# Kernel optimization log

Hardware: AMD Instinct MI355X
Metric: run time of the kernel (lower is better)

The kernel has to match this reference:

```python
import jax, jax.numpy as jnp
import numpy as np

TOKENS = 8192
DIM = 4096
N_EXPERTS = 256
TOPK = 8
N_GROUPS = 8
TOPK_GROUPS = 4
ROUTE_SCALE = 2.5


def setup_inputs() -> dict:
    key = jax.random.key(0)
    k1, k2, k3 = jax.random.split(key, 3)
    x = jax.random.normal(k1, (TOKENS, DIM), dtype=jnp.float32)
    W = jax.random.normal(k2, (N_EXPERTS, DIM), dtype=jnp.float32) * (DIM ** -0.5)
    bias = jax.random.normal(k3, (N_EXPERTS,), dtype=jnp.float32) * 0.01
    return {"x": x, "W": W, "bias": bias}


def reference(x, W, bias):
    T = x.shape[0]
    # linear scoring: [T, E]
    logits = jnp.einsum("td,ed->te", x, W)
    scores = jax.nn.sigmoid(logits)  # score_func == 'sigmoid'
    original_scores = scores
    s = scores + bias  # bias-corrected scores used only for routing
    # group-limited routing: [T, G, E/G]
    sg = s.reshape(T, N_GROUPS, -1)
    # bias is not None -> group score = sum of top-2 within each group
    group_scores = jax.lax.top_k(sg, 2)[0].sum(axis=-1)  # [T, G]
    gidx = jax.lax.top_k(group_scores, TOPK_GROUPS)[1]  # [T, topk_groups]
    mask = jnp.zeros((T, N_GROUPS), dtype=s.dtype).at[
        jnp.arange(T)[:, None], gidx
    ].set(1.0)
    s_masked = (sg * mask[:, :, None]).reshape(T, -1)  # [T, E]
    # final top-k over masked scores
    indices = jax.lax.top_k(s_masked, TOPK)[1]  # [T, topk] int32
    weights = jnp.take_along_axis(original_scores, indices, axis=1)
    # sigmoid path: renormalize selected weights
    weights = weights / weights.sum(axis=-1, keepdims=True)
    weights = weights * ROUTE_SCALE
    return weights.astype(x.dtype), indices
```

## Files before the change

### kernel.cpp

```cpp
#include <hip/hip_runtime.h>
#include <math.h>

#define TOKENS 8192
#define DIM 4096
#define NEXP 256
#define TK 8
#define ROUTE_SCALE 2.5f
#define TH1 1e-5f
#define TH2 2e-5f

#define PITCH 40

typedef _Float16 half8 __attribute__((ext_vector_type(8)));
typedef float f4 __attribute__((ext_vector_type(4)));
union H8 { half8 v; int4 q; };

__global__ __launch_bounds__(256) void wsplit(const float* __restrict__ W,
                                              _Float16* __restrict__ Whp,
                                              _Float16* __restrict__ Wlp,
                                              float4* __restrict__ Wt4,
                                              int* __restrict__ flag_cnt) {
    int fi = blockIdx.x * 256 + threadIdx.x;
    if (fi == 0) *flag_cnt = 0;
    int lane = fi & 63;
    int kc = (fi >> 6) & 127;
    int et = fi >> 13;
    int e = et * 16 + (lane & 15);
    int k = kc * 32 + ((lane >> 4) << 3);
    const float* src = W + (size_t)e * DIM + k;
    float4 a = *(const float4*)src;
    float4 b = *(const float4*)(src + 4);
    int kq = kc * 8 + ((lane >> 4) << 1);
    Wt4[(size_t)kq * NEXP + e] = a;
    Wt4[(size_t)(kq + 1) * NEXP + e] = b;
    float f[8] = {a.x, a.y, a.z, a.w, b.x, b.y, b.z, b.w};
    H8 hh, hl;
#pragma unroll
    for (int j = 0; j < 8; j++) {
        float ws = f[j] * 256.0f;
        _Float16 h = (_Float16)ws;
        float r = ws - (float)h;
        hh.v[j] = h;
        hl.v[j] = (_Float16)(r * 2048.0f);
    }
    *(int4*)(Whp + (size_t)fi * 8) = hh.q;
    *(int4*)(Wlp + (size_t)fi * 8) = hl.q;
}

__global__ __launch_bounds__(256, 3) void score_gemm(const float* __restrict__ x,
                                                     const _Float16* __restrict__ Whp,
                                                     const _Float16* __restrict__ Wlp,
                                                     float* __restrict__ parts) {
    __shared__ __align__(16) _Float16 sAh[2][64 * PITCH];
    __shared__ __align__(16) _Float16 sAl[2][64 * PITCH];

    const int m0 = blockIdx.x * 64;
    const int nb = blockIdx.y;
    const int chunk = blockIdx.z;
    const int kcb = 43 * chunk;
    const int kce = kcb + (chunk == 2 ? 42 : 43);

    const int tid = threadIdx.x;
    const int lane = tid & 63;
    const int wave = tid >> 6;
    const int et0 = nb * 8 + wave * 2;

    const int srow = tid >> 2;
    const int scol = (tid & 3) * 8;
    const int sidx = srow * PITCH + scol;
    const float* xrow = x + (size_t)(m0 + srow) * DIM + scol;

    f4 accH[4][2], accC[4][2];
#pragma unroll
    for (int i = 0; i < 4; i++)
#pragma unroll
        for (int j = 0; j < 2; j++) { accH[i][j] = (f4)0.0f; accC[i][j] = (f4)0.0f; }

    float4 ra[2][2];
    half8 bh[2][2], bl[2][2];

#define LOADRAW(S, KC)                                                         \
    {                                                                          \
        const float* p_ = xrow + (size_t)(KC) * 32;                            \
        ra[S][0] = *(const float4*)p_;                                         \
        ra[S][1] = *(const float4*)(p_ + 4);                                   \
    }

#define CONV(S, B_)                                                            \
    {                                                                          \
        float f_[8] = {ra[S][0].x, ra[S][0].y, ra[S][0].z, ra[S][0].w,         \
                       ra[S][1].x, ra[S][1].y, ra[S][1].z, ra[S][1].w};        \
        H8 hh_, hl_;                                                           \
        _Pragma("unroll") for (int j_ = 0; j_ < 8; j_++) {                     \
            float xv_ = f_[j_] * 16.0f;                                        \
            _Float16 hv_ = (_Float16)xv_;                                      \
            float r_ = xv_ - (float)hv_;                                       \
            hh_.v[j_] = hv_;                                                   \
            hl_.v[j_] = (_Float16)(r_ * 2048.0f);                              \
        }                                                                      \
        *(int4*)&sAh[B_][sidx] = hh_.q;                                        \
        *(int4*)&sAl[B_][sidx] = hl_.q;                                        \
    }

#define BLOAD(P_, KC)                                                          \
    _Pragma("unroll") for (int nt_ = 0; nt_ < 2; nt_++) {                      \
        size_t o_ = ((size_t)((et0 + nt_) * 128 + (KC)) * 64 + lane) * 8;      \
        bh[P_][nt_] = *(const half8*)(Whp + o_);                               \
        bl[P_][nt_] = *(const half8*)(Wlp + o_);                               \
    }

#define MFMA_PHASE(P)                                                          \
    _Pragma("unroll") for (int mt_ = 0; mt_ < 4; mt_++) {                      \
        int ra_ = (mt_ * 16 + (lane & 15)) * PITCH + ((lane >> 4) << 3);       \
        half8 ah_ = *(const half8*)&sAh[P][ra_];                               \
        half8 al_ = *(const half8*)&sAl[P][ra_];                               \
        _Pragma("unroll") for (int nt_ = 0; nt_ < 2; nt_++) {                  \
            accH[mt_][nt_] = __builtin_amdgcn_mfma_f32_16x16x32_f16(           \
                ah_, bh[P][nt_], accH[mt_][nt_], 0, 0, 0);                     \
            accC[mt_][nt_] = __builtin_amdgcn_mfma_f32_16x16x32_f16(           \
                ah_, bl[P][nt_], accC[mt_][nt_], 0, 0, 0);                     \
            accC[mt_][nt_] = __builtin_amdgcn_mfma_f32_16x16x32_f16(           \
                al_, bh[P][nt_], accC[mt_][nt_], 0, 0, 0);                     \
        }                                                                      \
    }

#define BARRIER() asm volatile("s_waitcnt lgkmcnt(0)\n\ts_barrier" ::: "memory")

#define ITER(KC, P)                                                            \
    {                                                                          \
        if ((KC) + 1 < kce) { BLOAD(P ^ 1, (KC) + 1) }                         \
        if ((KC) + 2 < kce) { LOADRAW(P, (KC) + 2) }                           \
        MFMA_PHASE(P)                                                          \
        if ((KC) + 1 < kce) { CONV(P ^ 1, P ^ 1) }                             \
        BARRIER();                                                             \
    }

    LOADRAW(0, kcb)
    CONV(0, 0)
    LOADRAW(1, kcb + 1)
    BLOAD(0, kcb)
    BARRIER();

    int kc = kcb;
    while (kc + 2 <= kce) {
        ITER(kc, 0)
        ITER(kc + 1, 1)
        kc += 2;
    }
    if (kc < kce) { ITER(kc, 0) }

    float* pc = parts + (size_t)chunk * TOKENS * NEXP;
#pragma unroll
    for (int mt = 0; mt < 4; mt++)
#pragma unroll
        for (int nt = 0; nt < 2; nt++) {
            int m = m0 + mt * 16 + ((lane >> 4) << 2);
            int e = (et0 + nt) * 16 + (lane & 15);
#pragma unroll
            for (int r = 0; r < 4; r++)
                pc[(size_t)(m + r) * NEXP + e] =
                    accH[mt][nt][r] + accC[mt][nt][r] * (1.0f / 2048.0f);
        }
#undef LOADRAW
#undef CONV
#undef BLOAD
#undef MFMA_PHASE
#undef BARRIER
#undef ITER
}

__global__ __launch_bounds__(256) void route_kernel(const float* __restrict__ parts,
                                                    const float* __restrict__ bias,
                                                    float* __restrict__ out_w,
                                                    float* __restrict__ out_i,
                                                    int* __restrict__ flag_cnt,
                                                    int* __restrict__ flag_list) {
    const int t = blockIdx.x * 4 + (threadIdx.x >> 6);
    const int l = threadIdx.x & 63;

    const float* p = parts + (size_t)t * NEXP + (l << 2);
    float4 q0 = *(const float4*)p;
    float4 q1 = *(const float4*)(p + (size_t)TOKENS * NEXP);
    float4 q2 = *(const float4*)(p + (size_t)2 * TOKENS * NEXP);
    float4 b4 = *(const float4*)&bias[l << 2];
    float sc[4], sb[4];
    {
        float lg0 = (q0.x + q1.x + q2.x) * (1.0f / 4096.0f);
        float lg1 = (q0.y + q1.y + q2.y) * (1.0f / 4096.0f);
        float lg2 = (q0.z + q1.z + q2.z) * (1.0f / 4096.0f);
        float lg3 = (q0.w + q1.w + q2.w) * (1.0f / 4096.0f);
        sc[0] = 1.0f / (1.0f + expf(-lg0));
        sc[1] = 1.0f / (1.0f + expf(-lg1));
        sc[2] = 1.0f / (1.0f + expf(-lg2));
        sc[3] = 1.0f / (1.0f + expf(-lg3));
        sb[0] = sc[0] + b4.x; sb[1] = sc[1] + b4.y;
        sb[2] = sc[2] + b4.z; sb[3] = sc[3] + b4.w;
    }

    float v1 = sb[0], v2 = -1e30f, v3 = -1e30f;
#pragma unroll
    for (int c = 1; c < 4; c++) {
        float xv = sb[c];
        if (xv > v1) { v3 = v2; v2 = v1; v1 = xv; }
        else if (xv > v2) { v3 = v2; v2 = xv; }
        else if (xv > v3) { v3 = xv; }
    }

#pragma unroll
    for (int m = 1; m < 8; m <<= 1) {
        float o1 = __shfl_xor(v1, m, 64);
        float o2 = __shfl_xor(v2, m, 64);
        float o3 = __shfl_xor(v3, m, 64);
        bool aw = (v1 >= o1);
        float A1 = aw ? v1 : o1, A2 = aw ? v2 : o2, A3 = aw ? v3 : o3;
        float B1 = aw ? o1 : v1, B2 = aw ? o2 : v2;
        float n2, n3;
        if (A2 >= B1) { n2 = A2; n3 = fmaxf(B1, A3); }
        else          { n2 = B1; n3 = fmaxf(A2, B2); }
        v1 = A1; v2 = n2; v3 = n3;
    }
    float gscore = v1 + v2;
    float gap23 = v2 - v3;
#pragma unroll
    for (int m = 8; m < 64; m <<= 1) gap23 = fminf(gap23, __shfl_xor(gap23, m, 64));

    float gs[8];
#pragma unroll
    for (int g = 0; g < 8; g++) gs[g] = __shfl(gscore, g << 3, 64);

    const int mygrp = l >> 3;
    int rank = 0;
#pragma unroll
    for (int g = 0; g < 8; g++) {
        bool better = (gs[g] > gscore) || (gs[g] == gscore && g < mygrp);
        rank += (g != mygrp && better) ? 1 : 0;
    }
    const bool sel = rank < 4;

    float minsel = 1e30f, maxuns = -1e30f;
#pragma unroll
    for (int g = 0; g < 8; g++) {
        int rg = 0;
#pragma unroll
        for (int g2 = 0; g2 < 8; g2++)
            rg += (g2 != g && ((gs[g2] > gs[g]) || (gs[g2] == gs[g] && g2 < g))) ? 1 : 0;
        if (rg < 4) minsel = fminf(minsel, gs[g]); else maxuns = fmaxf(maxuns, gs[g]);
    }
    float gap45 = minsel - maxuns;

    float cand[4];
#pragma unroll
    for (int c = 0; c < 4; c++) cand[c] = sel ? sb[c] : 0.0f;

    float wv[8], wi[8], vb[9];
    float wsum = 0.0f;
#pragma unroll
    for (int r = 0; r < 9; r++) {
        float v = cand[0];
        int idx = (l << 2);
#pragma unroll
        for (int c = 1; c < 4; c++) {
            if (cand[c] > v) { v = cand[c]; idx = (l << 2) + c; }
        }
#pragma unroll
        for (int m = 32; m >= 1; m >>= 1) {
            float ov = __shfl_xor(v, m, 64);
            int oi = __shfl_xor(idx, m, 64);
            if (ov > v || (ov == v && oi < idx)) { v = ov; idx = oi; }
        }
        vb[r] = v;
        if (r < 8) {
            const int cc = idx & 3;
            const bool own = (idx >> 2) == l;
            cand[0] = (own && cc == 0) ? -__builtin_inff() : cand[0];
            cand[1] = (own && cc == 1) ? -__builtin_inff() : cand[1];
            cand[2] = (own && cc == 2) ? -__builtin_inff() : cand[2];
            cand[3] = (own && cc == 3) ? -__builtin_inff() : cand[3];
            float tmp = (cc == 0) ? sc[0] : (cc == 1) ? sc[1] : (cc == 2) ? sc[2] : sc[3];
            float ws = __shfl(tmp, idx >> 2, 64);
            wv[r] = ws;
            wi[r] = (float)idx;
            wsum += ws;
        }
    }
    float mingap = 1e30f;
#pragma unroll
    for (int r = 0; r < 8; r++) mingap = fminf(mingap, vb[r] - vb[r + 1]);

    const float scale = ROUTE_SCALE / wsum;
    if (l == 0) {
        float* ow = out_w + (size_t)t * TK;
        float* oi = out_i + (size_t)t * TK;
#pragma unroll
        for (int r = 0; r < 8; r++) ow[r] = wv[r] * scale;
#pragma unroll
        for (int r = 0; r < 8; r++) oi[r] = wi[r];
        if (gap23 < TH1 || gap45 < TH2 || mingap < TH1) {
            int pos = atomicAdd(flag_cnt, 1);
            flag_list[pos] = t;
        }
    }
}

__global__ __launch_bounds__(256, 1) void fixup_kernel(const float* __restrict__ x,
                                                       const float4* __restrict__ Wt4,
                                                       const float* __restrict__ bias,
                                                       const int* __restrict__ flag_cnt,
                                                       const int* __restrict__ flag_list,
                                                       float* __restrict__ out_w,
                                                       float* __restrict__ out_i) {
    __shared__ float S[NEXP];
    __shared__ __align__(16) float sx[DIM];
    const int tid = threadIdx.x;

#define FILL(BUF, S_)                                                          \
    _Pragma("unroll") for (int q_ = 0; q_ < 8; q_++)                           \
        BUF[q_] = wt4r[(size_t)((S_) * 8 + q_) * NEXP];

#define CONSUME(BUF, S_)                                                       \
    {                                                                          \
        const float* xb_ = sx + (S_) * 32;                                     \
        _Pragma("unroll") for (int q_ = 0; q_ < 8; q_++) {                     \
            const float4 wv = BUF[q_];                                         \
            const float4 xv = *(const float4*)(xb_ + q_ * 4);                  \
            acc = fmaf(xv.x, wv.x, acc);                                       \
            acc = fmaf(xv.y, wv.y, acc);                                       \
            acc = fmaf(xv.z, wv.z, acc);                                       \
            acc = fmaf(xv.w, wv.w, acc);                                       \
        }                                                                      \
    }

    const int n = *flag_cnt;
    for (int i = blockIdx.x; i < n; i += gridDim.x) {
        const int t = flag_list[i];
        const float* xr = x + (size_t)t * DIM;
#pragma unroll
        for (int j = 0; j < 4; j++) {
            const int idx = (j * 256 + tid) * 4;
            *(float4*)&sx[idx] = *(const float4*)(xr + idx);
        }
        __syncthreads();

        const float4* wt4r = Wt4 + tid;
        float4 wb0[8], wb1[8], wb2[8], wb3[8];
        FILL(wb0, 0)
        FILL(wb1, 1)
        FILL(wb2, 2)
        FILL(wb3, 3)

        float acc = 0.0f;
        for (int c4 = 0; c4 < 31; c4++) {
            const int s = c4 * 4;
            CONSUME(wb0, s)
            FILL(wb0, s + 4)
            CONSUME(wb1, s + 1)
            FILL(wb1, s + 5)
            CONSUME(wb2, s + 2)
            FILL(wb2, s + 6)
            CONSUME(wb3, s + 3)
            FILL(wb3, s + 7)
        }
        CONSUME(wb0, 124)
        CONSUME(wb1, 125)
        CONSUME(wb2, 126)
        CONSUME(wb3, 127)

        S[tid] = 1.0f / (1.0f + expf(-acc));
        __syncthreads();
        if (tid < 64) {
            const int l = tid;
            float sc[4] = {S[4 * l], S[4 * l + 1], S[4 * l + 2], S[4 * l + 3]};
            float4 b4 = *(const float4*)&bias[4 * l];
            float sb[4] = {sc[0] + b4.x, sc[1] + b4.y, sc[2] + b4.z, sc[3] + b4.w};

            float h1 = fmaxf(sb[0], sb[1]), q1 = fminf(sb[0], sb[1]);
            float h2 = fmaxf(sb[2], sb[3]), q2 = fminf(sb[2], sb[3]);
            float m1 = fmaxf(h1, h2);
            float m2 = fmaxf(fminf(h1, h2), fmaxf(q1, q2));
#pragma unroll
            for (int m = 1; m < 8; m <<= 1) {
                float o1 = __shfl_xor(m1, m, 64);
                float o2 = __shfl_xor(m2, m, 64);
                float nm1 = fmaxf(m1, o1);
                float nm2 = fmaxf(fminf(m1, o1), fmaxf(m2, o2));
                m1 = nm1; m2 = nm2;
            }
            float gscore = m1 + m2;
            float gs[8];
#pragma unroll
            for (int g = 0; g < 8; g++) gs[g] = __shfl(gscore, g << 3, 64);
            const int mygrp = l >> 3;
            int rank = 0;
#pragma unroll
            for (int g = 0; g < 8; g++) {
                bool better = (gs[g] > gscore) || (gs[g] == gscore && g < mygrp);
                rank += (g != mygrp && better) ? 1 : 0;
            }
            const bool selg = rank < 4;
            float cand[4];
#pragma unroll
            for (int c = 0; c < 4; c++) cand[c] = selg ? sb[c] : 0.0f;
            float wv[8], wi[8];
            float wsum = 0.0f;
#pragma unroll
            for (int r = 0; r < 8; r++) {
                float v = cand[0];
                int idx = (l << 2);
#pragma unroll
                for (int c = 1; c < 4; c++) {
                    if (cand[c] > v) { v = cand[c]; idx = (l << 2) + c; }
                }
#pragma unroll
                for (int m = 32; m >= 1; m >>= 1) {
                    float ov = __shfl_xor(v, m, 64);
                    int oi = __shfl_xor(idx, m, 64);
                    if (ov > v || (ov == v && oi < idx)) { v = ov; idx = oi; }
                }
                const int cc = idx & 3;
                const bool own = (idx >> 2) == l;
                cand[0] = (own && cc == 0) ? -__builtin_inff() : cand[0];
                cand[1] = (own && cc == 1) ? -__builtin_inff() : cand[1];
                cand[2] = (own && cc == 2) ? -__builtin_inff() : cand[2];
                cand[3] = (own && cc == 3) ? -__builtin_inff() : cand[3];
                float tmp = (cc == 0) ? sc[0] : (cc == 1) ? sc[1] : (cc == 2) ? sc[2] : sc[3];
                float ws = __shfl(tmp, idx >> 2, 64);
                wv[r] = ws;
                wi[r] = (float)idx;
                wsum += ws;
            }
            const float scale = ROUTE_SCALE / wsum;
            if (l == 0) {
                float* ow = out_w + (size_t)t * TK;
                float* oi = out_i + (size_t)t * TK;
#pragma unroll
                for (int r = 0; r < 8; r++) ow[r] = wv[r] * scale;
#pragma unroll
                for (int r = 0; r < 8; r++) oi[r] = wi[r];
            }
        }
        __syncthreads();
    }
#undef FILL
#undef CONSUME
}

extern "C" void kernel_launch(void* const* d_in, const int* in_sizes, int n_in,
                              void* d_out, int out_size, void* d_ws, size_t ws_size,
                              hipStream_t stream) {
    const float* x = (const float*)d_in[0];
    const float* W = (const float*)d_in[1];
    const float* bias = (const float*)d_in[2];
    float* out = (float*)d_out;

    char* p = (char*)d_ws;
    float* parts = (float*)p;            p += (size_t)3 * TOKENS * NEXP * 4;
    _Float16* Whp = (_Float16*)p;        p += (size_t)NEXP * DIM * 2;
    _Float16* Wlp = (_Float16*)p;        p += (size_t)NEXP * DIM * 2;
    int* flag_cnt = (int*)p;
    int* flag_list = flag_cnt + 4;       p += 40960;
    float4* Wt4 = (float4*)p;

    wsplit<<<512, 256, 0, stream>>>(W, Whp, Wlp, Wt4, flag_cnt);

    dim3 gGemm(TOKENS / 64, 2, 3);
    score_gemm<<<gGemm, 256, 0, stream>>>(x, Whp, Wlp, parts);

    route_kernel<<<TOKENS / 4, 256, 0, stream>>>(parts, bias, out,
                                                 out + (size_t)TOKENS * TK,
                                                 flag_cnt, flag_list);
    fixup_kernel<<<256, 256, 0, stream>>>(x, Wt4, bias, flag_cnt, flag_list,
                                          out, out + (size_t)TOKENS * TK);
}
```

Measured before the change: 301.6 us.

## Cover all experts per GEMM block and batch four tokens in fixup

The score GEMM now uses 512-thread blocks whose 8 waves cover all 256 experts. Each x tile is loaded and split into fp16 hi/lo once per block instead of once per expert half, and the K dimension is split into 4 chunks of 32 rather than 3 uneven ones. The route kernel sums four partial buffers, which adds partial-sum memory traffic. The fixup kernel processes four flagged tokens per block, reusing each streamed W value across four dot products at the cost of more shared memory.

```diff
diff --git a/kernel.cpp b/kernel.cpp
--- a/kernel.cpp
+++ b/kernel.cpp
@@ -12,8 +12,10 @@
 #define PITCH 40
 
 typedef _Float16 half8 __attribute__((ext_vector_type(8)));
+typedef _Float16 half4 __attribute__((ext_vector_type(4)));
 typedef float f4 __attribute__((ext_vector_type(4)));
 union H8 { half8 v; int4 q; };
+union H4 { half4 v; int2 q; };
 
 __global__ __launch_bounds__(256) void wsplit(const float* __restrict__ W,
                                               _Float16* __restrict__ Whp,
@@ -47,7 +49,7 @@
     *(int4*)(Wlp + (size_t)fi * 8) = hl.q;
 }
 
-__global__ __launch_bounds__(256, 3) void score_gemm(const float* __restrict__ x,
+__global__ __launch_bounds__(512, 4) void score_gemm(const float* __restrict__ x,
                                                      const _Float16* __restrict__ Whp,
                                                      const _Float16* __restrict__ Wlp,
                                                      float* __restrict__ parts) {
@@ -55,18 +57,17 @@
     __shared__ __align__(16) _Float16 sAl[2][64 * PITCH];
 
     const int m0 = blockIdx.x * 64;
-    const int nb = blockIdx.y;
-    const int chunk = blockIdx.z;
-    const int kcb = 43 * chunk;
-    const int kce = kcb + (chunk == 2 ? 42 : 43);
+    const int chunk = blockIdx.y;
+    const int kcb = chunk * 32;
+    const int kce = kcb + 32;
 
     const int tid = threadIdx.x;
     const int lane = tid & 63;
     const int wave = tid >> 6;
-    const int et0 = nb * 8 + wave * 2;
-
-    const int srow = tid >> 2;
-    const int scol = (tid & 3) * 8;
+    const int et0 = wave * 2;
+
+    const int srow = tid >> 3;
+    const int scol = (tid & 7) * 4;
     const int sidx = srow * PITCH + scol;
     const float* xrow = x + (size_t)(m0 + srow) * DIM + scol;
 
@@ -76,30 +77,25 @@
 #pragma unroll
         for (int j = 0; j < 2; j++) { accH[i][j] = (f4)0.0f; accC[i][j] = (f4)0.0f; }
 
-    float4 ra[2][2];
+    float4 ra[2];
     half8 bh[2][2], bl[2][2];
 
 #define LOADRAW(S, KC)                                                         \
-    {                                                                          \
-        const float* p_ = xrow + (size_t)(KC) * 32;                            \
-        ra[S][0] = *(const float4*)p_;                                         \
-        ra[S][1] = *(const float4*)(p_ + 4);                                   \
-    }
+    { ra[S] = *(const float4*)(xrow + (size_t)(KC) * 32); }
 
 #define CONV(S, B_)                                                            \
     {                                                                          \
-        float f_[8] = {ra[S][0].x, ra[S][0].y, ra[S][0].z, ra[S][0].w,         \
-                       ra[S][1].x, ra[S][1].y, ra[S][1].z, ra[S][1].w};        \
-        H8 hh_, hl_;                                                           \
-        _Pragma("unroll") for (int j_ = 0; j_ < 8; j_++) {                     \
+        float f_[4] = {ra[S].x, ra[S].y, ra[S].z, ra[S].w};                    \
+        H4 hh_, hl_;                                                           \
+        _Pragma("unroll") for (int j_ = 0; j_ < 4; j_++) {                     \
             float xv_ = f_[j_] * 16.0f;                                        \
             _Float16 hv_ = (_Float16)xv_;                                      \
             float r_ = xv_ - (float)hv_;                                       \
             hh_.v[j_] = hv_;                                                   \
             hl_.v[j_] = (_Float16)(r_ * 2048.0f);                              \
         }                                                                      \
-        *(int4*)&sAh[B_][sidx] = hh_.q;                                        \
-        *(int4*)&sAl[B_][sidx] = hl_.q;                                        \
+        *(int2*)&sAh[B_][sidx] = hh_.q;                                        \
+        *(int2*)&sAl[B_][sidx] = hl_.q;                                        \
     }
 
 #define BLOAD(P_, KC)                                                          \
@@ -147,7 +143,6 @@
         ITER(kc + 1, 1)
         kc += 2;
     }
-    if (kc < kce) { ITER(kc, 0) }
 
     float* pc = parts + (size_t)chunk * TOKENS * NEXP;
 #pragma unroll
@@ -182,13 +177,14 @@
     float4 q0 = *(const float4*)p;
     float4 q1 = *(const float4*)(p + (size_t)TOKENS * NEXP);
     float4 q2 = *(const float4*)(p + (size_t)2 * TOKENS * NEXP);
+    float4 q3 = *(const float4*)(p + (size_t)3 * TOKENS * NEXP);
     float4 b4 = *(const float4*)&bias[l << 2];
     float sc[4], sb[4];
     {
-        float lg0 = (q0.x + q1.x + q2.x) * (1.0f / 4096.0f);
-        float lg1 = (q0.y + q1.y + q2.y) * (1.0f / 4096.0f);
-        float lg2 = (q0.z + q1.z + q2.z) * (1.0f / 4096.0f);
-        float lg3 = (q0.w + q1.w + q2.w) * (1.0f / 4096.0f);
+        float lg0 = (q0.x + q1.x + q2.x + q3.x) * (1.0f / 4096.0f);
+        float lg1 = (q0.y + q1.y + q2.y + q3.y) * (1.0f / 4096.0f);
+        float lg2 = (q0.z + q1.z + q2.z + q3.z) * (1.0f / 4096.0f);
+        float lg3 = (q0.w + q1.w + q2.w + q3.w) * (1.0f / 4096.0f);
         sc[0] = 1.0f / (1.0f + expf(-lg0));
         sc[1] = 1.0f / (1.0f + expf(-lg1));
         sc[2] = 1.0f / (1.0f + expf(-lg2));
@@ -309,35 +305,49 @@
                                                        const int* __restrict__ flag_list,
                                                        float* __restrict__ out_w,
                                                        float* __restrict__ out_i) {
-    __shared__ float S[NEXP];
-    __shared__ __align__(16) float sx[DIM];
+    __shared__ float S[4][NEXP];
+    __shared__ __align__(16) float sx[4][DIM];
     const int tid = threadIdx.x;
 
 #define FILL(BUF, S_)                                                          \
     _Pragma("unroll") for (int q_ = 0; q_ < 8; q_++)                           \
         BUF[q_] = wt4r[(size_t)((S_) * 8 + q_) * NEXP];
 
-#define CONSUME(BUF, S_)                                                       \
+#define CONSUME4(BUF, S_)                                                      \
     {                                                                          \
-        const float* xb_ = sx + (S_) * 32;                                     \
         _Pragma("unroll") for (int q_ = 0; q_ < 8; q_++) {                     \
             const float4 wv = BUF[q_];                                         \
-            const float4 xv = *(const float4*)(xb_ + q_ * 4);                  \
-            acc = fmaf(xv.x, wv.x, acc);                                       \
-            acc = fmaf(xv.y, wv.y, acc);                                       \
-            acc = fmaf(xv.z, wv.z, acc);                                       \
-            acc = fmaf(xv.w, wv.w, acc);                                       \
+            const float4 x0 = *(const float4*)&sx[0][(S_) * 32 + q_ * 4];      \
+            const float4 x1 = *(const float4*)&sx[1][(S_) * 32 + q_ * 4];      \
+            const float4 x2 = *(const float4*)&sx[2][(S_) * 32 + q_ * 4];      \
+            const float4 x3 = *(const float4*)&sx[3][(S_) * 32 + q_ * 4];      \
+            a0 = fmaf(x0.x, wv.x, a0); a0 = fmaf(x0.y, wv.y, a0);              \
+            a0 = fmaf(x0.z, wv.z, a0); a0 = fmaf(x0.w, wv.w, a0);              \
+            a1 = fmaf(x1.x, wv.x, a1); a1 = fmaf(x1.y, wv.y, a1);              \
+            a1 = fmaf(x1.z, wv.z, a1); a1 = fmaf(x1.w, wv.w, a1);              \
+            a2 = fmaf(x2.x, wv.x, a2); a2 = fmaf(x2.y, wv.y, a2);              \
+            a2 = fmaf(x2.z, wv.z, a2); a2 = fmaf(x2.w, wv.w, a2);              \
+            a3 = fmaf(x3.x, wv.x, a3); a3 = fmaf(x3.y, wv.y, a3);              \
+            a3 = fmaf(x3.z, wv.z, a3); a3 = fmaf(x3.w, wv.w, a3);              \
         }                                                                      \
     }
 
     const int n = *flag_cnt;
-    for (int i = blockIdx.x; i < n; i += gridDim.x) {
-        const int t = flag_list[i];
-        const float* xr = x + (size_t)t * DIM;
+    for (int base = blockIdx.x * 4; base < n; base += gridDim.x * 4) {
+        int tt[4];
 #pragma unroll
         for (int j = 0; j < 4; j++) {
-            const int idx = (j * 256 + tid) * 4;
-            *(float4*)&sx[idx] = *(const float4*)(xr + idx);
+            int ii = base + j;
+            tt[j] = flag_list[ii < n ? ii : n - 1];
+        }
+#pragma unroll
+        for (int j = 0; j < 4; j++) {
+            const float* xr = x + (size_t)tt[j] * DIM;
+#pragma unroll
+            for (int q = 0; q < 4; q++) {
+                const int idx = (q * 256 + tid) * 4;
+                *(float4*)&sx[j][idx] = *(const float4*)(xr + idx);
+            }
         }
         __syncthreads();
 
@@ -348,28 +358,35 @@
         FILL(wb2, 2)
         FILL(wb3, 3)
 
-        float acc = 0.0f;
+        float a0 = 0.0f, a1 = 0.0f, a2 = 0.0f, a3 = 0.0f;
         for (int c4 = 0; c4 < 31; c4++) {
             const int s = c4 * 4;
-            CONSUME(wb0, s)
+            CONSUME4(wb0, s)
             FILL(wb0, s + 4)
-            CONSUME(wb1, s + 1)
+            CONSUME4(wb1, s + 1)
             FILL(wb1, s + 5)
-            CONSUME(wb2, s + 2)
+            CONSUME4(wb2, s + 2)
             FILL(wb2, s + 6)
-            CONSUME(wb3, s + 3)
+            CONSUME4(wb3, s + 3)
             FILL(wb3, s + 7)
         }
-        CONSUME(wb0, 124)
-        CONSUME(wb1, 125)
-        CONSUME(wb2, 126)
-        CONSUME(wb3, 127)
-
-        S[tid] = 1.0f / (1.0f + expf(-acc));
+        CONSUME4(wb0, 124)
+        CONSUME4(wb1, 125)
+        CONSUME4(wb2, 126)
+        CONSUME4(wb3, 127)
+
+        S[0][tid] = 1.0f / (1.0f + expf(-a0));
+        S[1][tid] = 1.0f / (1.0f + expf(-a1));
+        S[2][tid] = 1.0f / (1.0f + expf(-a2));
+        S[3][tid] = 1.0f / (1.0f + expf(-a3));
         __syncthreads();
-        if (tid < 64) {
-            const int l = tid;
-            float sc[4] = {S[4 * l], S[4 * l + 1], S[4 * l + 2], S[4 * l + 3]};
+
+        {
+            const int w = tid >> 6;
+            const int l = tid & 63;
+            const bool valid = (base + w) < n;
+            const int t = tt[w];
+            float sc[4] = {S[w][4 * l], S[w][4 * l + 1], S[w][4 * l + 2], S[w][4 * l + 3]};
             float4 b4 = *(const float4*)&bias[4 * l];
             float sb[4] = {sc[0] + b4.x, sc[1] + b4.y, sc[2] + b4.z, sc[3] + b4.w};
 
@@ -429,7 +446,7 @@
                 wsum += ws;
             }
             const float scale = ROUTE_SCALE / wsum;
-            if (l == 0) {
+            if (valid && l == 0) {
                 float* ow = out_w + (size_t)t * TK;
                 float* oi = out_i + (size_t)t * TK;
 #pragma unroll
@@ -441,7 +458,7 @@
         __syncthreads();
     }
 #undef FILL
-#undef CONSUME
+#undef CONSUME4
 }
 
 extern "C" void kernel_launch(void* const* d_in, const int* in_sizes, int n_in,
@@ -453,7 +470,7 @@
     float* out = (float*)d_out;
 
     char* p = (char*)d_ws;
-    float* parts = (float*)p;            p += (size_t)3 * TOKENS * NEXP * 4;
+    float* parts = (float*)p;            p += (size_t)4 * TOKENS * NEXP * 4;
     _Float16* Whp = (_Float16*)p;        p += (size_t)NEXP * DIM * 2;
     _Float16* Wlp = (_Float16*)p;        p += (size_t)NEXP * DIM * 2;
     int* flag_cnt = (int*)p;
@@ -462,8 +479,8 @@
 
     wsplit<<<512, 256, 0, stream>>>(W, Whp, Wlp, Wt4, flag_cnt);
 
-    dim3 gGemm(TOKENS / 64, 2, 3);
-    score_gemm<<<gGemm, 256, 0, stream>>>(x, Whp, Wlp, parts);
+    dim3 gGemm(TOKENS / 64, 4);
+    score_gemm<<<gGemm, 512, 0, stream>>>(x, Whp, Wlp, parts);
 
     route_kernel<<<TOKENS / 4, 256, 0, stream>>>(parts, bias, out,
                                                  out + (size_t)TOKENS * TK,
```

Result: slower. 408.8 us (+35.6%).

## Widen GEMM block to cover all experts and split K into four chunks

Applied to the files above, without the earlier changes.

The score GEMM block grows from 256 to 512 threads, and its 8 waves now cover all 256 experts, so the two expert halves no longer each reload and re-convert the same x tile. This cuts the redundant global reads of x and the duplicated fp32-to-split-fp16 conversion work. The K split changes from three uneven chunks to four chunks of 32, so the route kernel now sums four partial buffers. That raises partial-sum traffic and workspace size in exchange. Each thread now loads and converts 4 floats instead of 8.

```diff
diff --git a/kernel.cpp b/kernel.cpp
--- a/kernel.cpp
+++ b/kernel.cpp
@@ -12,8 +12,10 @@
 #define PITCH 40
 
 typedef _Float16 half8 __attribute__((ext_vector_type(8)));
+typedef _Float16 half4 __attribute__((ext_vector_type(4)));
 typedef float f4 __attribute__((ext_vector_type(4)));
 union H8 { half8 v; int4 q; };
+union H4 { half4 v; int2 q; };
 
 __global__ __launch_bounds__(256) void wsplit(const float* __restrict__ W,
                                               _Float16* __restrict__ Whp,
@@ -47,7 +49,7 @@
     *(int4*)(Wlp + (size_t)fi * 8) = hl.q;
 }
 
-__global__ __launch_bounds__(256, 3) void score_gemm(const float* __restrict__ x,
+__global__ __launch_bounds__(512, 4) void score_gemm(const float* __restrict__ x,
                                                      const _Float16* __restrict__ Whp,
                                                      const _Float16* __restrict__ Wlp,
                                                      float* __restrict__ parts) {
@@ -55,18 +57,17 @@
     __shared__ __align__(16) _Float16 sAl[2][64 * PITCH];
 
     const int m0 = blockIdx.x * 64;
-    const int nb = blockIdx.y;
-    const int chunk = blockIdx.z;
-    const int kcb = 43 * chunk;
-    const int kce = kcb + (chunk == 2 ? 42 : 43);
+    const int chunk = blockIdx.y;
+    const int kcb = chunk * 32;
+    const int kce = kcb + 32;
 
     const int tid = threadIdx.x;
     const int lane = tid & 63;
     const int wave = tid >> 6;
-    const int et0 = nb * 8 + wave * 2;
-
-    const int srow = tid >> 2;
-    const int scol = (tid & 3) * 8;
+    const int et0 = wave * 2;
+
+    const int srow = tid >> 3;
+    const int scol = (tid & 7) * 4;
     const int sidx = srow * PITCH + scol;
     const float* xrow = x + (size_t)(m0 + srow) * DIM + scol;
 
@@ -76,30 +77,25 @@
 #pragma unroll
         for (int j = 0; j < 2; j++) { accH[i][j] = (f4)0.0f; accC[i][j] = (f4)0.0f; }
 
-    float4 ra[2][2];
+    float4 ra[2];
     half8 bh[2][2], bl[2][2];
 
 #define LOADRAW(S, KC)                                                         \
-    {                                                                          \
-        const float* p_ = xrow + (size_t)(KC) * 32;                            \
-        ra[S][0] = *(const float4*)p_;                                         \
-        ra[S][1] = *(const float4*)(p_ + 4);                                   \
-    }
+    { ra[S] = *(const float4*)(xrow + (size_t)(KC) * 32); }
 
 #define CONV(S, B_)                                                            \
     {                                                                          \
-        float f_[8] = {ra[S][0].x, ra[S][0].y, ra[S][0].z, ra[S][0].w,         \
-                       ra[S][1].x, ra[S][1].y, ra[S][1].z, ra[S][1].w};        \
-        H8 hh_, hl_;                                                           \
-        _Pragma("unroll") for (int j_ = 0; j_ < 8; j_++) {                     \
+        float f_[4] = {ra[S].x, ra[S].y, ra[S].z, ra[S].w};                    \
+        H4 hh_, hl_;                                                           \
+        _Pragma("unroll") for (int j_ = 0; j_ < 4; j_++) {                     \
             float xv_ = f_[j_] * 16.0f;                                        \
             _Float16 hv_ = (_Float16)xv_;                                      \
             float r_ = xv_ - (float)hv_;                                       \
             hh_.v[j_] = hv_;                                                   \
             hl_.v[j_] = (_Float16)(r_ * 2048.0f);                              \
         }                                                                      \
-        *(int4*)&sAh[B_][sidx] = hh_.q;                                        \
-        *(int4*)&sAl[B_][sidx] = hl_.q;                                        \
+        *(int2*)&sAh[B_][sidx] = hh_.q;                                        \
+        *(int2*)&sAl[B_][sidx] = hl_.q;                                        \
     }
 
 #define BLOAD(P_, KC)                                                          \
@@ -147,7 +143,6 @@
         ITER(kc + 1, 1)
         kc += 2;
     }
-    if (kc < kce) { ITER(kc, 0) }
 
     float* pc = parts + (size_t)chunk * TOKENS * NEXP;
 #pragma unroll
@@ -182,13 +177,14 @@
     float4 q0 = *(const float4*)p;
     float4 q1 = *(const float4*)(p + (size_t)TOKENS * NEXP);
     float4 q2 = *(const float4*)(p + (size_t)2 * TOKENS * NEXP);
+    float4 q3 = *(const float4*)(p + (size_t)3 * TOKENS * NEXP);
     float4 b4 = *(const float4*)&bias[l << 2];
     float sc[4], sb[4];
     {
-        float lg0 = (q0.x + q1.x + q2.x) * (1.0f / 4096.0f);
-        float lg1 = (q0.y + q1.y + q2.y) * (1.0f / 4096.0f);
-        float lg2 = (q0.z + q1.z + q2.z) * (1.0f / 4096.0f);
-        float lg3 = (q0.w + q1.w + q2.w) * (1.0f / 4096.0f);
+        float lg0 = (q0.x + q1.x + q2.x + q3.x) * (1.0f / 4096.0f);
+        float lg1 = (q0.y + q1.y + q2.y + q3.y) * (1.0f / 4096.0f);
+        float lg2 = (q0.z + q1.z + q2.z + q3.z) * (1.0f / 4096.0f);
+        float lg3 = (q0.w + q1.w + q2.w + q3.w) * (1.0f / 4096.0f);
         sc[0] = 1.0f / (1.0f + expf(-lg0));
         sc[1] = 1.0f / (1.0f + expf(-lg1));
         sc[2] = 1.0f / (1.0f + expf(-lg2));
@@ -453,7 +449,7 @@
     float* out = (float*)d_out;
 
     char* p = (char*)d_ws;
-    float* parts = (float*)p;            p += (size_t)3 * TOKENS * NEXP * 4;
+    float* parts = (float*)p;            p += (size_t)4 * TOKENS * NEXP * 4;
     _Float16* Whp = (_Float16*)p;        p += (size_t)NEXP * DIM * 2;
     _Float16* Wlp = (_Float16*)p;        p += (size_t)NEXP * DIM * 2;
     int* flag_cnt = (int*)p;
@@ -462,8 +458,8 @@
 
     wsplit<<<512, 256, 0, stream>>>(W, Whp, Wlp, Wt4, flag_cnt);
 
-    dim3 gGemm(TOKENS / 64, 2, 3);
-    score_gemm<<<gGemm, 256, 0, stream>>>(x, Whp, Wlp, parts);
+    dim3 gGemm(TOKENS / 64, 4);
+    score_gemm<<<gGemm, 512, 0, stream>>>(x, Whp, Wlp, parts);
 
     route_kernel<<<TOKENS / 4, 256, 0, stream>>>(parts, bias, out,
                                                  out + (size_t)TOKENS * TK,
```

Result: slower. 320.4 us (+6.2%).

## Batch four flagged tokens per block in fixup to reuse W loads

Applied to the files above, without the earlier changes.

The fixup kernel now handles four flagged tokens per block instead of one. Each W float4 fetched is reused across four dot products, x is read straight from global memory (uniform broadcast loads) instead of being staged in LDS, and all four wavefronts run the routing logic, one token each. The grid grows from 256 to 512 blocks. This cuts the W bandwidth per flagged token, at the cost of more registers for the extra accumulators and x loads that are no longer staged through LDS.

```diff
diff --git a/kernel.cpp b/kernel.cpp
--- a/kernel.cpp
+++ b/kernel.cpp
@@ -302,44 +302,51 @@
     }
 }
 
-__global__ __launch_bounds__(256, 1) void fixup_kernel(const float* __restrict__ x,
-                                                       const float4* __restrict__ Wt4,
-                                                       const float* __restrict__ bias,
-                                                       const int* __restrict__ flag_cnt,
-                                                       const int* __restrict__ flag_list,
-                                                       float* __restrict__ out_w,
-                                                       float* __restrict__ out_i) {
-    __shared__ float S[NEXP];
-    __shared__ __align__(16) float sx[DIM];
+__global__ __launch_bounds__(256, 1) void fixup_fused(const float* __restrict__ x,
+                                                      const float4* __restrict__ Wt4,
+                                                      const float* __restrict__ bias,
+                                                      const int* __restrict__ flag_cnt,
+                                                      const int* __restrict__ flag_list,
+                                                      float* __restrict__ out_w,
+                                                      float* __restrict__ out_i) {
+    __shared__ float S[4][NEXP];
     const int tid = threadIdx.x;
 
 #define FILL(BUF, S_)                                                          \
     _Pragma("unroll") for (int q_ = 0; q_ < 8; q_++)                           \
         BUF[q_] = wt4r[(size_t)((S_) * 8 + q_) * NEXP];
 
-#define CONSUME(BUF, S_)                                                       \
+#define CONSUME4(BUF, S_)                                                      \
     {                                                                          \
-        const float* xb_ = sx + (S_) * 32;                                     \
         _Pragma("unroll") for (int q_ = 0; q_ < 8; q_++) {                     \
             const float4 wv = BUF[q_];                                         \
-            const float4 xv = *(const float4*)(xb_ + q_ * 4);                  \
-            acc = fmaf(xv.x, wv.x, acc);                                       \
-            acc = fmaf(xv.y, wv.y, acc);                                       \
-            acc = fmaf(xv.z, wv.z, acc);                                       \
-            acc = fmaf(xv.w, wv.w, acc);                                       \
+            const float4 xv0 = *(const float4*)(x0p + (S_) * 32 + q_ * 4);     \
+            const float4 xv1 = *(const float4*)(x1p + (S_) * 32 + q_ * 4);     \
+            const float4 xv2 = *(const float4*)(x2p + (S_) * 32 + q_ * 4);     \
+            const float4 xv3 = *(const float4*)(x3p + (S_) * 32 + q_ * 4);     \
+            a0 = fmaf(xv0.x, wv.x, a0); a0 = fmaf(xv0.y, wv.y, a0);            \
+            a0 = fmaf(xv0.z, wv.z, a0); a0 = fmaf(xv0.w, wv.w, a0);            \
+            a1 = fmaf(xv1.x, wv.x, a1); a1 = fmaf(xv1.y, wv.y, a1);            \
+            a1 = fmaf(xv1.z, wv.z, a1); a1 = fmaf(xv1.w, wv.w, a1);            \
+            a2 = fmaf(xv2.x, wv.x, a2); a2 = fmaf(xv2.y, wv.y, a2);            \
+            a2 = fmaf(xv2.z, wv.z, a2); a2 = fmaf(xv2.w, wv.w, a2);            \
+            a3 = fmaf(xv3.x, wv.x, a3); a3 = fmaf(xv3.y, wv.y, a3);            \
+            a3 = fmaf(xv3.z, wv.z, a3); a3 = fmaf(xv3.w, wv.w, a3);            \
         }                                                                      \
     }
 
     const int n = *flag_cnt;
-    for (int i = blockIdx.x; i < n; i += gridDim.x) {
-        const int t = flag_list[i];
-        const float* xr = x + (size_t)t * DIM;
+    for (int base = blockIdx.x * 4; base < n; base += gridDim.x * 4) {
+        int tt[4];
 #pragma unroll
         for (int j = 0; j < 4; j++) {
-            const int idx = (j * 256 + tid) * 4;
-            *(float4*)&sx[idx] = *(const float4*)(xr + idx);
-        }
-        __syncthreads();
+            int ii = base + j;
+            tt[j] = flag_list[ii < n ? ii : n - 1];
+        }
+        const float* x0p = x + (size_t)tt[0] * DIM;
+        const float* x1p = x + (size_t)tt[1] * DIM;
+        const float* x2p = x + (size_t)tt[2] * DIM;
+        const float* x3p = x + (size_t)tt[3] * DIM;
 
         const float4* wt4r = Wt4 + tid;
         float4 wb0[8], wb1[8], wb2[8], wb3[8];
@@ -348,28 +355,35 @@
         FILL(wb2, 2)
         FILL(wb3, 3)
 
-        float acc = 0.0f;
+        float a0 = 0.0f, a1 = 0.0f, a2 = 0.0f, a3 = 0.0f;
         for (int c4 = 0; c4 < 31; c4++) {
             const int s = c4 * 4;
-            CONSUME(wb0, s)
+            CONSUME4(wb0, s)
             FILL(wb0, s + 4)
-            CONSUME(wb1, s + 1)
+            CONSUME4(wb1, s + 1)
             FILL(wb1, s + 5)
-            CONSUME(wb2, s + 2)
+            CONSUME4(wb2, s + 2)
             FILL(wb2, s + 6)
-            CONSUME(wb3, s + 3)
+            CONSUME4(wb3, s + 3)
             FILL(wb3, s + 7)
         }
-        CONSUME(wb0, 124)
-        CONSUME(wb1, 125)
-        CONSUME(wb2, 126)
-        CONSUME(wb3, 127)
-
-        S[tid] = 1.0f / (1.0f + expf(-acc));
+        CONSUME4(wb0, 124)
+        CONSUME4(wb1, 125)
+        CONSUME4(wb2, 126)
+        CONSUME4(wb3, 127)
+
+        S[0][tid] = 1.0f / (1.0f + expf(-a0));
+        S[1][tid] = 1.0f / (1.0f + expf(-a1));
+        S[2][tid] = 1.0f / (1.0f + expf(-a2));
+        S[3][tid] = 1.0f / (1.0f + expf(-a3));
         __syncthreads();
-        if (tid < 64) {
-            const int l = tid;
-            float sc[4] = {S[4 * l], S[4 * l + 1], S[4 * l + 2], S[4 * l + 3]};
+
+        {
+            const int w = tid >> 6;
+            const int l = tid & 63;
+            const bool valid = (base + w) < n;
+            const int t = tt[w];
+            float sc[4] = {S[w][4 * l], S[w][4 * l + 1], S[w][4 * l + 2], S[w][4 * l + 3]};
             float4 b4 = *(const float4*)&bias[4 * l];
             float sb[4] = {sc[0] + b4.x, sc[1] + b4.y, sc[2] + b4.z, sc[3] + b4.w};
 
@@ -429,7 +443,7 @@
                 wsum += ws;
             }
             const float scale = ROUTE_SCALE / wsum;
-            if (l == 0) {
+            if (valid && l == 0) {
                 float* ow = out_w + (size_t)t * TK;
                 float* oi = out_i + (size_t)t * TK;
 #pragma unroll
@@ -441,7 +455,7 @@
         __syncthreads();
     }
 #undef FILL
-#undef CONSUME
+#undef CONSUME4
 }
 
 extern "C" void kernel_launch(void* const* d_in, const int* in_sizes, int n_in,
@@ -468,6 +482,6 @@
     route_kernel<<<TOKENS / 4, 256, 0, stream>>>(parts, bias, out,
                                                  out + (size_t)TOKENS * TK,
                                                  flag_cnt, flag_list);
-    fixup_kernel<<<256, 256, 0, stream>>>(x, Wt4, bias, flag_cnt, flag_list,
-                                          out, out + (size_t)TOKENS * TK);
+    fixup_fused<<<512, 256, 0, stream>>>(x, Wt4, bias, flag_cnt, flag_list,
+                                         out, out + (size_t)TOKENS * TK);
 }
```

Result: slower. 411.5 us (+36.5%).
